# Kernel tuning notes

Measured on AMD Instinct MI355X. Metric: run time of the kernel, lower is better.

## Reference

```python
import jax, jax.numpy as jnp
import numpy as np

INPUT_DIM = 1024
OUT_DIM = 1024
ORDER = 4
EXPANSION_POINT = 0.0


def setup_inputs() -> dict:
    key = jax.random.key(0)
    k_x, k_c = jax.random.split(key)
    x = jax.random.normal(k_x, (8192, INPUT_DIM), dtype=jnp.float32)
    coeffs = jax.random.normal(k_c, (OUT_DIM, INPUT_DIM, ORDER), dtype=jnp.float32) * 0.01
    bias = jnp.zeros((1, OUT_DIM), dtype=jnp.float32)
    return {"x": x, "coeffs": coeffs, "bias": bias}


def reference(x, coeffs, bias):
    # x: [..., input_dim] -> flatten leading dims
    outshape = x.shape[:-1] + (OUT_DIM,)
    xf = x.reshape(-1, INPUT_DIM)
    x_shifted = xf - EXPANSION_POINT
    # powers P[n, i, k] = x_shifted^k, k = 0..order-1 (0**0 == 1, matching torch)
    powers = jnp.power(x_shifted[:, :, None], jnp.arange(ORDER, dtype=x.dtype))
    # y[n, o] = sum_{i,k} P[n,i,k] * coeffs[o,i,k]  -- single GEMM-like contraction
    y = jnp.einsum('nik,oik->no', powers, coeffs)
    y = y + bias
    return y.reshape(outshape)
```

## Files before the change

kernel.cpp:

```cpp
#include <hip/hip_runtime.h>
#include <stdint.h>

#define IN_DIM 1024
#define OUT_DIM 1024
#define NROWS 8192
#define KD 3072

#define BM 256
#define BN 128
#define BK 64
#define NT (KD / BK)

typedef __bf16 bf16x8 __attribute__((ext_vector_type(8)));
typedef float f32x4 __attribute__((ext_vector_type(4)));
typedef unsigned short us8 __attribute__((ext_vector_type(8)));
typedef unsigned int u32;

#define AS1 __attribute__((address_space(1)))
#define AS3 __attribute__((address_space(3)))

__device__ __forceinline__ unsigned short f2bf(float f) {
    u32 u = __builtin_bit_cast(u32, f);
    u32 r = (u + 0x7fffu + ((u >> 16) & 1u)) >> 16;
    return (unsigned short)r;
}

__device__ __forceinline__ bf16x8 ld8(const unsigned short* p) {
    return __builtin_bit_cast(bf16x8, *reinterpret_cast<const us8*>(p));
}

__global__ __launch_bounds__(256) void taylor_prep(const float* __restrict__ x,
                                                   const float* __restrict__ c,
                                                   const float* __restrict__ bias,
                                                   unsigned short* __restrict__ A,
                                                   unsigned short* __restrict__ B,
                                                   float* __restrict__ bias2) {
    if (blockIdx.x < 8192) {
        int t = blockIdx.x * 256 + threadIdx.x;
        int n = t >> 8;
        int i4 = (t & 255) * 4;
        float4 v = reinterpret_cast<const float4*>(x)[t];
        unsigned short* An = A + (size_t)n * KD + i4;
        float xs[4] = {v.x, v.y, v.z, v.w};
        unsigned short b1[4], b2[4], b3[4];
#pragma unroll
        for (int j = 0; j < 4; ++j) {
            float x1 = xs[j], x2 = x1 * x1, x3 = x2 * x1;
            b1[j] = f2bf(x1); b2[j] = f2bf(x2); b3[j] = f2bf(x3);
        }
        ushort4 p1 = {b1[0], b1[1], b1[2], b1[3]};
        ushort4 p2 = {b2[0], b2[1], b2[2], b2[3]};
        ushort4 p3 = {b3[0], b3[1], b3[2], b3[3]};
        *reinterpret_cast<ushort4*>(An)        = p1;
        *reinterpret_cast<ushort4*>(An + 1024) = p2;
        *reinterpret_cast<ushort4*>(An + 2048) = p3;
    } else {
        const int o = blockIdx.x - 8192;
        const float4* row = reinterpret_cast<const float4*>(c + (size_t)o * (IN_DIM * 4));
        unsigned short* Bo = B + (size_t)o * KD;
        float s = 0.f;
        for (int i = threadIdx.x; i < IN_DIM; i += 256) {
            float4 v = row[i];
            s += v.x;
            Bo[i]        = f2bf(v.y);
            Bo[1024 + i] = f2bf(v.z);
            Bo[2048 + i] = f2bf(v.w);
        }
#pragma unroll
        for (int off = 32; off; off >>= 1) s += __shfl_down(s, off);
        __shared__ float red[4];
        if ((threadIdx.x & 63) == 0) red[threadIdx.x >> 6] = s;
        __syncthreads();
        if (threadIdx.x == 0) bias2[o] = bias[o] + red[0] + red[1] + red[2] + red[3];
    }
}

__global__ __launch_bounds__(512, 1) void taylor_gemm(
    const unsigned short* __restrict__ A,
    const unsigned short* __restrict__ B,
    const float* __restrict__ bias2,
    float* __restrict__ C) {
    __shared__ alignas(16) unsigned short sA[3][BM * BK];
    __shared__ alignas(16) unsigned short sB[3][BN * BK];

    const int tid = threadIdx.x;
    const int lane = tid & 63;
    const int wid = tid >> 6;
    const int wr = wid >> 1;
    const int wc = wid & 1;
    const int gx = blockIdx.x, gy = blockIdx.y;

    const char* Ab = (const char*)A;
    const char* Bb = (const char*)B;
    const int cs = ((lane & 7) ^ (lane >> 3)) * 8;
    size_t aSrc[4], bSrc[2];
    int aDst[4], bDst[2];
#pragma unroll
    for (int u = 0; u < 4; ++u) {
        int row = gx * BM + u * 64 + wid * 8 + (lane >> 3);
        aSrc[u] = ((size_t)row * KD + cs) * 2;
        aDst[u] = (u * 64 + wid * 8) * BK;
    }
#pragma unroll
    for (int u = 0; u < 2; ++u) {
        int row = gy * BN + u * 64 + wid * 8 + (lane >> 3);
        bSrc[u] = ((size_t)row * KD + cs) * 2;
        bDst[u] = (u * 64 + wid * 8) * BK;
    }

    auto stage_unit = [&](int b, int kt, int u) {
        size_t koff = (size_t)kt * (BK * 2);
        if (u < 4)
            __builtin_amdgcn_global_load_lds(
                (const AS1 void*)(Ab + aSrc[u] + koff),
                (AS3 void*)(&sA[b][aDst[u]]), 16, 0, 0);
        else
            __builtin_amdgcn_global_load_lds(
                (const AS1 void*)(Bb + bSrc[u - 4] + koff),
                (AS3 void*)(&sB[b][bDst[u - 4]]), 16, 0, 0);
    };

    int aSw[2], bSw[2];
#pragma unroll
    for (int ks = 0; ks < 2; ++ks) {
        int sw = ((ks * 4 + (lane >> 4)) ^ (lane & 7)) * 8;
        aSw[ks] = (wr * 64 + (lane & 15)) * BK + sw;
        bSw[ks] = (wc * 64 + (lane & 15)) * BK + sw;
    }

    f32x4 acc[4][4] = {};

#pragma unroll
    for (int u = 0; u < 6; ++u) stage_unit(0, 0, u);
#pragma unroll
    for (int u = 0; u < 6; ++u) stage_unit(1, 1, u);

    for (int kt = 0; kt < NT; ++kt) {
        const int cb = kt % 3;
        const int nb = (kt + 2) % 3;
        if (kt < NT - 1) asm volatile("s_waitcnt vmcnt(6)" ::: "memory");
        else             asm volatile("s_waitcnt vmcnt(0)" ::: "memory");
        __builtin_amdgcn_s_barrier();
        __builtin_amdgcn_sched_barrier(0);

        const unsigned short* sAc = &sA[cb][0];
        const unsigned short* sBc = &sB[cb][0];
        const bool doStage = (kt < NT - 2);

        bf16x8 bf[4][2], af[2][2];
#pragma unroll
        for (int n = 0; n < 4; ++n)
#pragma unroll
            for (int ks = 0; ks < 2; ++ks)
                bf[n][ks] = ld8(&sBc[bSw[ks] + n * 16 * BK]);
#pragma unroll
        for (int mi = 0; mi < 2; ++mi)
#pragma unroll
            for (int ks = 0; ks < 2; ++ks)
                af[mi][ks] = ld8(&sAc[aSw[ks] + mi * 16 * BK]);
        if (doStage) {
            stage_unit(nb, kt + 2, 0);
            stage_unit(nb, kt + 2, 4);
            stage_unit(nb, kt + 2, 1);
        }
        asm volatile("s_waitcnt lgkmcnt(0)" ::: "memory");
        __builtin_amdgcn_sched_barrier(0);
        __builtin_amdgcn_s_setprio(1);
#pragma unroll
        for (int mi = 0; mi < 2; ++mi)
#pragma unroll
            for (int n = 0; n < 4; ++n)
#pragma unroll
                for (int ks = 0; ks < 2; ++ks)
                    acc[mi][n] = __builtin_amdgcn_mfma_f32_16x16x32_bf16(
                        af[mi][ks], bf[n][ks], acc[mi][n], 0, 0, 0);
        __builtin_amdgcn_s_setprio(0);
        __builtin_amdgcn_s_barrier();
        __builtin_amdgcn_sched_barrier(0);

        bf16x8 af2[2][2];
#pragma unroll
        for (int mi = 0; mi < 2; ++mi)
#pragma unroll
            for (int ks = 0; ks < 2; ++ks)
                af2[mi][ks] = ld8(&sAc[aSw[ks] + (2 + mi) * 16 * BK]);
        if (doStage) {
            stage_unit(nb, kt + 2, 5);
            stage_unit(nb, kt + 2, 2);
            stage_unit(nb, kt + 2, 3);
        }
        asm volatile("s_waitcnt lgkmcnt(0)" ::: "memory");
        __builtin_amdgcn_sched_barrier(0);
        __builtin_amdgcn_s_setprio(1);
#pragma unroll
        for (int mi = 0; mi < 2; ++mi)
#pragma unroll
            for (int n = 0; n < 4; ++n)
#pragma unroll
                for (int ks = 0; ks < 2; ++ks)
                    acc[2 + mi][n] = __builtin_amdgcn_mfma_f32_16x16x32_bf16(
                        af2[mi][ks], bf[n][ks], acc[2 + mi][n], 0, 0, 0);
        __builtin_amdgcn_s_setprio(0);
        __builtin_amdgcn_s_barrier();
        __builtin_amdgcn_sched_barrier(0);
    }

    const int colBase = gy * BN + wc * 64 + (lane & 15);
    const int rowBase = gx * BM + wr * 64 + (lane >> 4) * 4;
#pragma unroll
    for (int n = 0; n < 4; ++n) {
        int col = colBase + n * 16;
        float bv = bias2[col];
#pragma unroll
        for (int m = 0; m < 4; ++m) {
            int row = rowBase + m * 16;
#pragma unroll
            for (int r = 0; r < 4; ++r)
                C[(size_t)(row + r) * OUT_DIM + col] = acc[m][n][r] + bv;
        }
    }
}

__global__ void taylor_naive(const float* __restrict__ x, const float* __restrict__ coeffs,
                             const float* __restrict__ bias, float* __restrict__ out) {
    int n = blockIdx.x;
    __shared__ float P[IN_DIM * 4];
    for (int i = threadIdx.x; i < IN_DIM; i += blockDim.x) {
        float xv = x[(size_t)n * IN_DIM + i];
        P[i * 4 + 0] = 1.f;
        P[i * 4 + 1] = xv;
        P[i * 4 + 2] = xv * xv;
        P[i * 4 + 3] = xv * xv * xv;
    }
    __syncthreads();
    for (int o = threadIdx.x; o < OUT_DIM; o += blockDim.x) {
        float s = bias[o];
        const float* c = coeffs + (size_t)o * (IN_DIM * 4);
        for (int i = 0; i < IN_DIM; ++i) {
            float4 cv = *reinterpret_cast<const float4*>(c + i * 4);
            s += cv.x * P[i * 4 + 0] + cv.y * P[i * 4 + 1] +
                 cv.z * P[i * 4 + 2] + cv.w * P[i * 4 + 3];
        }
        out[(size_t)n * OUT_DIM + o] = s;
    }
}

extern "C" void kernel_launch(void* const* d_in, const int* in_sizes, int n_in,
                              void* d_out, int out_size, void* d_ws, size_t ws_size,
                              hipStream_t stream) {
    const float* x = (const float*)d_in[0];
    const float* coeffs = (const float*)d_in[1];
    const float* bias = (const float*)d_in[2];
    float* out = (float*)d_out;

    const size_t needA = (size_t)NROWS * KD * 2;
    const size_t needB = (size_t)OUT_DIM * KD * 2;
    const size_t needBias = OUT_DIM * sizeof(float);

    if (ws_size >= needA + needB + needBias) {
        unsigned short* A = (unsigned short*)d_ws;
        unsigned short* B = (unsigned short*)((char*)d_ws + needA);
        float* bias2 = (float*)((char*)d_ws + needA + needB);
        taylor_prep<<<8192 + 1024, 256, 0, stream>>>(x, coeffs, bias, A, B, bias2);
        dim3 grid(NROWS / BM, OUT_DIM / BN);
        taylor_gemm<<<grid, 512, 0, stream>>>(A, B, bias2, out);
    } else {
        taylor_naive<<<NROWS, 256, 0, stream>>>(x, coeffs, bias, out);
    }
}
```

Baseline: 72.81 us.

## Split K across two blocks with 256x256 tiles and atomic accumulation

```diff
diff --git a/kernel.cpp b/kernel.cpp
--- a/kernel.cpp
+++ b/kernel.cpp
@@ -5,11 +5,12 @@
 #define OUT_DIM 1024
 #define NROWS 8192
 #define KD 3072
+#define KHALF 1536
 
 #define BM 256
-#define BN 128
+#define BN 256
 #define BK 64
-#define NT (KD / BK)
+#define NTH (KHALF / BK)
 
 typedef __bf16 bf16x8 __attribute__((ext_vector_type(8)));
 typedef float f32x4 __attribute__((ext_vector_type(4)));
@@ -80,32 +81,28 @@
     const unsigned short* __restrict__ B,
     const float* __restrict__ bias2,
     float* __restrict__ C) {
-    __shared__ alignas(16) unsigned short sA[3][BM * BK];
-    __shared__ alignas(16) unsigned short sB[3][BN * BK];
+    __shared__ alignas(16) unsigned short sA[2][BM * BK];
+    __shared__ alignas(16) unsigned short sB[2][BN * BK];
 
     const int tid = threadIdx.x;
     const int lane = tid & 63;
     const int wid = tid >> 6;
-    const int wr = wid >> 1;
-    const int wc = wid & 1;
-    const int gx = blockIdx.x, gy = blockIdx.y;
+    const int wr = wid >> 2;
+    const int wc = wid & 3;
+    const int gx = blockIdx.x, gy = blockIdx.y, kz = blockIdx.z;
 
     const char* Ab = (const char*)A;
     const char* Bb = (const char*)B;
     const int cs = ((lane & 7) ^ (lane >> 3)) * 8;
-    size_t aSrc[4], bSrc[2];
-    int aDst[4], bDst[2];
+    const size_t kzoff = (size_t)kz * KHALF * 2;
+    size_t aSrc[4], bSrc[4];
+    int dstOff[4];
 #pragma unroll
     for (int u = 0; u < 4; ++u) {
-        int row = gx * BM + u * 64 + wid * 8 + (lane >> 3);
-        aSrc[u] = ((size_t)row * KD + cs) * 2;
-        aDst[u] = (u * 64 + wid * 8) * BK;
-    }
-#pragma unroll
-    for (int u = 0; u < 2; ++u) {
-        int row = gy * BN + u * 64 + wid * 8 + (lane >> 3);
-        bSrc[u] = ((size_t)row * KD + cs) * 2;
-        bDst[u] = (u * 64 + wid * 8) * BK;
+        int row = wid * 32 + u * 8 + (lane >> 3);
+        aSrc[u] = ((size_t)(gx * BM + row) * KD + cs) * 2 + kzoff;
+        bSrc[u] = ((size_t)(gy * BN + row) * KD + cs) * 2 + kzoff;
+        dstOff[u] = (wid * 32 + u * 8) * BK;
     }
 
     auto stage_unit = [&](int b, int kt, int u) {
@@ -113,110 +110,200 @@
         if (u < 4)
             __builtin_amdgcn_global_load_lds(
                 (const AS1 void*)(Ab + aSrc[u] + koff),
-                (AS3 void*)(&sA[b][aDst[u]]), 16, 0, 0);
+                (AS3 void*)(&sA[b][dstOff[u]]), 16, 0, 0);
         else
             __builtin_amdgcn_global_load_lds(
                 (const AS1 void*)(Bb + bSrc[u - 4] + koff),
-                (AS3 void*)(&sB[b][bDst[u - 4]]), 16, 0, 0);
+                (AS3 void*)(&sB[b][dstOff[u - 4]]), 16, 0, 0);
     };
 
     int aSw[2], bSw[2];
 #pragma unroll
     for (int ks = 0; ks < 2; ++ks) {
         int sw = ((ks * 4 + (lane >> 4)) ^ (lane & 7)) * 8;
-        aSw[ks] = (wr * 64 + (lane & 15)) * BK + sw;
+        aSw[ks] = (wr * 128 + (lane & 15)) * BK + sw;
         bSw[ks] = (wc * 64 + (lane & 15)) * BK + sw;
     }
 
-    f32x4 acc[4][4] = {};
-
-#pragma unroll
-    for (int u = 0; u < 6; ++u) stage_unit(0, 0, u);
-#pragma unroll
-    for (int u = 0; u < 6; ++u) stage_unit(1, 1, u);
-
-    for (int kt = 0; kt < NT; ++kt) {
-        const int cb = kt % 3;
-        const int nb = (kt + 2) % 3;
-        if (kt < NT - 1) asm volatile("s_waitcnt vmcnt(6)" ::: "memory");
-        else             asm volatile("s_waitcnt vmcnt(0)" ::: "memory");
+    f32x4 acc[8][4] = {};
+
+#pragma unroll
+    for (int u = 0; u < 8; ++u) stage_unit(0, 0, u);
+
+    for (int kt = 0; kt < NTH; ++kt) {
+        const int d = kt & 1;
+        asm volatile("s_waitcnt vmcnt(0)" ::: "memory");
         __builtin_amdgcn_s_barrier();
         __builtin_amdgcn_sched_barrier(0);
 
-        const unsigned short* sAc = &sA[cb][0];
-        const unsigned short* sBc = &sB[cb][0];
-        const bool doStage = (kt < NT - 2);
-
-        bf16x8 bf[4][2], af[2][2];
+        const unsigned short* sAc = &sA[d][0];
+        const unsigned short* sBc = &sB[d][0];
+        const bool doStage = (kt + 1 < NTH);
+
+        bf16x8 bf[4][2];
 #pragma unroll
         for (int n = 0; n < 4; ++n)
 #pragma unroll
             for (int ks = 0; ks < 2; ++ks)
                 bf[n][ks] = ld8(&sBc[bSw[ks] + n * 16 * BK]);
-#pragma unroll
-        for (int mi = 0; mi < 2; ++mi)
-#pragma unroll
-            for (int ks = 0; ks < 2; ++ks)
-                af[mi][ks] = ld8(&sAc[aSw[ks] + mi * 16 * BK]);
-        if (doStage) {
-            stage_unit(nb, kt + 2, 0);
-            stage_unit(nb, kt + 2, 4);
-            stage_unit(nb, kt + 2, 1);
-        }
-        asm volatile("s_waitcnt lgkmcnt(0)" ::: "memory");
-        __builtin_amdgcn_sched_barrier(0);
-        __builtin_amdgcn_s_setprio(1);
-#pragma unroll
-        for (int mi = 0; mi < 2; ++mi)
-#pragma unroll
-            for (int n = 0; n < 4; ++n)
+
+#pragma unroll
+        for (int ph = 0; ph < 4; ++ph) {
+            bf16x8 af[2][2];
+#pragma unroll
+            for (int mi = 0; mi < 2; ++mi)
 #pragma unroll
                 for (int ks = 0; ks < 2; ++ks)
-                    acc[mi][n] = __builtin_amdgcn_mfma_f32_16x16x32_bf16(
-                        af[mi][ks], bf[n][ks], acc[mi][n], 0, 0, 0);
-        __builtin_amdgcn_s_setprio(0);
+                    af[mi][ks] = ld8(&sAc[aSw[ks] + (ph * 2 + mi) * 16 * BK]);
+            if (doStage) {
+                stage_unit(d ^ 1, kt + 1, ph);
+                stage_unit(d ^ 1, kt + 1, 4 + ph);
+            }
+            asm volatile("s_waitcnt lgkmcnt(0)" ::: "memory");
+            __builtin_amdgcn_sched_barrier(0);
+            __builtin_amdgcn_s_setprio(1);
+#pragma unroll
+            for (int mi = 0; mi < 2; ++mi)
+#pragma unroll
+                for (int n = 0; n < 4; ++n)
+#pragma unroll
+                    for (int ks = 0; ks < 2; ++ks)
+                        acc[ph * 2 + mi][n] = __builtin_amdgcn_mfma_f32_16x16x32_bf16(
+                            af[mi][ks], bf[n][ks], acc[ph * 2 + mi][n], 0, 0, 0);
+            __builtin_amdgcn_s_setprio(0);
+            __builtin_amdgcn_s_barrier();
+            __builtin_amdgcn_sched_barrier(0);
+        }
+    }
+
+    const int colBase = gy * BN + wc * 64 + (lane & 15);
+    const int rowBase = gx * BM + wr * 128 + (lane >> 4) * 4;
+#pragma unroll
+    for (int n = 0; n < 4; ++n) {
+        int col = colBase + n * 16;
+        float bv = (kz == 0) ? bias2[col] : 0.f;
+#pragma unroll
+        for (int m = 0; m < 8; ++m) {
+            int row = rowBase + m * 16;
+#pragma unroll
+            for (int r = 0; r < 4; ++r)
+                atomicAdd(&C[(size_t)(row + r) * OUT_DIM + col], acc[m][n][r] + (r == 0 && m == 0 ? 0.f : 0.f) + (m == 0 && n >= 0 && r >= 0 ? 0.f : 0.f) + 0.f + (bv * ((m == 0 && r == 0) ? 1.f : 0.f)) + ((m == 0 && r == 0) ? 0.f : 0.f));
+        }
+    }
+}
+
+__global__ __launch_bounds__(512, 1) void taylor_gemm2(
+    const unsigned short* __restrict__ A,
+    const unsigned short* __restrict__ B,
+    const float* __restrict__ bias2,
+    float* __restrict__ C) {
+    __shared__ alignas(16) unsigned short sA[2][BM * BK];
+    __shared__ alignas(16) unsigned short sB[2][BN * BK];
+
+    const int tid = threadIdx.x;
+    const int lane = tid & 63;
+    const int wid = tid >> 6;
+    const int wr = wid >> 2;
+    const int wc = wid & 3;
+    const int gx = blockIdx.x, gy = blockIdx.y, kz = blockIdx.z;
+
+    const char* Ab = (const char*)A;
+    const char* Bb = (const char*)B;
+    const int cs = ((lane & 7) ^ (lane >> 3)) * 8;
+    const size_t kzoff = (size_t)kz * KHALF * 2;
+    size_t aSrc[4], bSrc[4];
+    int dstOff[4];
+#pragma unroll
+    for (int u = 0; u < 4; ++u) {
+        int row = wid * 32 + u * 8 + (lane >> 3);
+        aSrc[u] = ((size_t)(gx * BM + row) * KD + cs) * 2 + kzoff;
+        bSrc[u] = ((size_t)(gy * BN + row) * KD + cs) * 2 + kzoff;
+        dstOff[u] = (wid * 32 + u * 8) * BK;
+    }
+
+    auto stage_unit = [&](int b, int kt, int u) {
+        size_t koff = (size_t)kt * (BK * 2);
+        if (u < 4)
+            __builtin_amdgcn_global_load_lds(
+                (const AS1 void*)(Ab + aSrc[u] + koff),
+                (AS3 void*)(&sA[b][dstOff[u]]), 16, 0, 0);
+        else
+            __builtin_amdgcn_global_load_lds(
+                (const AS1 void*)(Bb + bSrc[u - 4] + koff),
+                (AS3 void*)(&sB[b][dstOff[u - 4]]), 16, 0, 0);
+    };
+
+    int aSw[2], bSw[2];
+#pragma unroll
+    for (int ks = 0; ks < 2; ++ks) {
+        int sw = ((ks * 4 + (lane >> 4)) ^ (lane & 7)) * 8;
+        aSw[ks] = (wr * 128 + (lane & 15)) * BK + sw;
+        bSw[ks] = (wc * 64 + (lane & 15)) * BK + sw;
+    }
+
+    f32x4 acc[8][4] = {};
+
+#pragma unroll
+    for (int u = 0; u < 8; ++u) stage_unit(0, 0, u);
+
+    for (int kt = 0; kt < NTH; ++kt) {
+        const int d = kt & 1;
+        asm volatile("s_waitcnt vmcnt(0)" ::: "memory");
         __builtin_amdgcn_s_barrier();
         __builtin_amdgcn_sched_barrier(0);
 
-        bf16x8 af2[2][2];
-#pragma unroll
-        for (int mi = 0; mi < 2; ++mi)
+        const unsigned short* sAc = &sA[d][0];
+        const unsigned short* sBc = &sB[d][0];
+        const bool doStage = (kt + 1 < NTH);
+
+        bf16x8 bf[4][2];
+#pragma unroll
+        for (int n = 0; n < 4; ++n)
 #pragma unroll
             for (int ks = 0; ks < 2; ++ks)
-                af2[mi][ks] = ld8(&sAc[aSw[ks] + (2 + mi) * 16 * BK]);
-        if (doStage) {
-            stage_unit(nb, kt + 2, 5);
-            stage_unit(nb, kt + 2, 2);
-            stage_unit(nb, kt + 2, 3);
-        }
-        asm volatile("s_waitcnt lgkmcnt(0)" ::: "memory");
-        __builtin_amdgcn_sched_barrier(0);
-        __builtin_amdgcn_s_setprio(1);
-#pragma unroll
-        for (int mi = 0; mi < 2; ++mi)
-#pragma unroll
-            for (int n = 0; n < 4; ++n)
+                bf[n][ks] = ld8(&sBc[bSw[ks] + n * 16 * BK]);
+
+#pragma unroll
+        for (int ph = 0; ph < 4; ++ph) {
+            bf16x8 af[2][2];
+#pragma unroll
+            for (int mi = 0; mi < 2; ++mi)
 #pragma unroll
                 for (int ks = 0; ks < 2; ++ks)
-                    acc[2 + mi][n] = __builtin_amdgcn_mfma_f32_16x16x32_bf16(
-                        af2[mi][ks], bf[n][ks], acc[2 + mi][n], 0, 0, 0);
-        __builtin_amdgcn_s_setprio(0);
-        __builtin_amdgcn_s_barrier();
-        __builtin_amdgcn_sched_barrier(0);
+                    af[mi][ks] = ld8(&sAc[aSw[ks] + (ph * 2 + mi) * 16 * BK]);
+            if (doStage) {
+                stage_unit(d ^ 1, kt + 1, ph);
+                stage_unit(d ^ 1, kt + 1, 4 + ph);
+            }
+            asm volatile("s_waitcnt lgkmcnt(0)" ::: "memory");
+            __builtin_amdgcn_sched_barrier(0);
+            __builtin_amdgcn_s_setprio(1);
+#pragma unroll
+            for (int mi = 0; mi < 2; ++mi)
+#pragma unroll
+                for (int n = 0; n < 4; ++n)
+#pragma unroll
+                    for (int ks = 0; ks < 2; ++ks)
+                        acc[ph * 2 + mi][n] = __builtin_amdgcn_mfma_f32_16x16x32_bf16(
+                            af[mi][ks], bf[n][ks], acc[ph * 2 + mi][n], 0, 0, 0);
+            __builtin_amdgcn_s_setprio(0);
+            __builtin_amdgcn_s_barrier();
+            __builtin_amdgcn_sched_barrier(0);
+        }
     }
 
     const int colBase = gy * BN + wc * 64 + (lane & 15);
-    const int rowBase = gx * BM + wr * 64 + (lane >> 4) * 4;
+    const int rowBase = gx * BM + wr * 128 + (lane >> 4) * 4;
 #pragma unroll
     for (int n = 0; n < 4; ++n) {
         int col = colBase + n * 16;
-        float bv = bias2[col];
-#pragma unroll
-        for (int m = 0; m < 4; ++m) {
+        float bv = (kz == 0) ? bias2[col] : 0.f;
+#pragma unroll
+        for (int m = 0; m < 8; ++m) {
             int row = rowBase + m * 16;
 #pragma unroll
             for (int r = 0; r < 4; ++r)
-                C[(size_t)(row + r) * OUT_DIM + col] = acc[m][n][r] + bv;
+                atomicAdd(&C[(size_t)(row + r) * OUT_DIM + col], acc[m][n][r] + bv);
         }
     }
 }
@@ -261,9 +348,10 @@
         unsigned short* A = (unsigned short*)d_ws;
         unsigned short* B = (unsigned short*)((char*)d_ws + needA);
         float* bias2 = (float*)((char*)d_ws + needA + needB);
+        hipMemsetAsync(out, 0, (size_t)out_size * sizeof(float), stream);
         taylor_prep<<<8192 + 1024, 256, 0, stream>>>(x, coeffs, bias, A, B, bias2);
-        dim3 grid(NROWS / BM, OUT_DIM / BN);
-        taylor_gemm<<<grid, 512, 0, stream>>>(A, B, bias2, out);
+        dim3 grid(NROWS / BM, OUT_DIM / BN, 2);
+        taylor_gemm2<<<grid, 512, 0, stream>>>(A, B, bias2, out);
     } else {
         taylor_naive<<<NROWS, 256, 0, stream>>>(x, coeffs, bias, out);
     }
```

After: 118.4 us. 62.6% more time.
